# Optimization experiments

Hardware: AMD Instinct MI355X
Metric: run time of the kernel (lower is better)

The kernel has to match this reference:

```python
import jax, jax.numpy as jnp
import numpy as np

N = 50000
F = 128
E = 800000
HOP = 3
ALPHA = 0.2  # leaky relu slope


def setup_inputs() -> dict:
    key = jax.random.key(0)
    ks = jax.random.split(key, 6)
    x = jax.random.normal(ks[0], (N, F), dtype=jnp.float32)
    h0 = jax.random.normal(ks[1], (N, F), dtype=jnp.float32)
    edge_index = jax.random.randint(ks[2], (2, E), 0, N, dtype=jnp.int32)
    edge_weight = jax.random.uniform(ks[3], (E,), dtype=jnp.float32)
    # xavier-uniform-ish params
    lim_w = float(np.sqrt(6.0 / (F + F)))
    W_att = jax.random.uniform(ks[4], (F, F), dtype=jnp.float32, minval=-lim_w, maxval=lim_w)
    lim_a = 1.414 * float(np.sqrt(6.0 / (2 * F + 1)))
    a = jax.random.uniform(ks[5], (2 * F, 1), dtype=jnp.float32, minval=-lim_a, maxval=lim_a)
    temp = jnp.zeros((4,), dtype=jnp.float32)
    return {"x": x, "h0": h0, "edge_index": edge_index, "edge_weight": edge_weight,
            "W_att": W_att, "a": a, "temp": temp}


def _segment_softmax(e, rows, num_segments):
    m = jax.ops.segment_max(e, rows, num_segments=num_segments)
    m = jnp.where(jnp.isfinite(m), m, 0.0)  # guard empty rows
    ex = jnp.exp(e - m[rows])
    s = jax.ops.segment_sum(ex, rows, num_segments=num_segments)
    s = jnp.where(s > 0, s, 1.0)
    return ex / s[rows]


def reference(x, h0, edge_index, edge_weight, W_att, a, temp):
    rows, cols = edge_index[0], edge_index[1]
    # --- attention (edge-wise, never materializing dense NxN e) ---
    feat = x @ W_att                       # [N, F]
    f1 = (feat @ a[:F]).squeeze(-1)        # [N]
    f2 = (feat @ a[F:]).squeeze(-1)        # [N]
    e = f1[rows] + f2[cols]                # e[i,j] at edges
    e = jnp.where(e > 0, e, ALPHA * e)     # leaky relu
    att = _segment_softmax(e, rows, N)     # sparse row softmax values
    P = 0.5 * att
    # --- lifting bases ---
    coe = jax.nn.sigmoid(temp)
    rowsum = jax.ops.segment_sum(edge_weight * P, rows, num_segments=N)  # [N]
    update = x
    feat_prime = None
    for step in range(HOP):
        # sparse mm: U @ update
        update = jax.ops.segment_sum(att[:, None] * update[cols], rows, num_segments=N)
        feat_even = coe[0] * x + update
        feat_odd = update - feat_even * rowsum[:, None]
        feat_prime = feat_odd if step == 0 else coe[2] * feat_prime + (1.0 - coe[2]) * feat_odd
    return feat_prime
```

## Files before the change

### kernel.cpp

```cpp
#include <hip/hip_runtime.h>
#include <hip/hip_fp16.h>

#define NN 50000
#define FF 128
#define EE 800000
#define ALPHA 0.2f
#define ESHIFT 4.0f

#define NBINS 196
#define CAPB 5120
#define EPB 2048
#define NWIN 784
#define WCAP 1600

__global__ void k_w(const float* __restrict__ W, const float* __restrict__ a,
                    float* __restrict__ w12) {
    int k = threadIdx.x;
    float s1 = 0.f, s2 = 0.f;
    const float* wr = W + k * FF;
    for (int j = 0; j < FF; ++j) {
        float w = wr[j];
        s1 += w * a[j];
        s2 += w * a[FF + j];
    }
    w12[k] = s1;
    w12[FF + k] = s2;
}

__global__ void k_f(const float* __restrict__ x, const float* __restrict__ w12,
                    float* __restrict__ f1, float* __restrict__ f2,
                    __half* __restrict__ xh) {
    int gid = blockIdx.x * blockDim.x + threadIdx.x;
    int node = gid >> 6;
    int lane = threadIdx.x & 63;
    if (node >= NN) return;
    float2 xv = ((const float2*)(x + (size_t)node * FF))[lane];
    ((__half2*)(xh + (size_t)node * FF))[lane] = __float22half2_rn(xv);
    float2 w1 = ((const float2*)w12)[lane];
    float2 w2 = ((const float2*)(w12 + FF))[lane];
    float s1 = xv.x * w1.x + xv.y * w1.y;
    float s2 = xv.x * w2.x + xv.y * w2.y;
#pragma unroll
    for (int o = 32; o > 0; o >>= 1) {
        s1 += __shfl_down(s1, o);
        s2 += __shfl_down(s2, o);
    }
    if (lane == 0) { f1[node] = s1; f2[node] = s2; }
}

__global__ void k_bin(const int* __restrict__ rows, const int* __restrict__ cols,
                      const float* __restrict__ ew, const float* __restrict__ f1,
                      const float* __restrict__ f2, int* __restrict__ bin_fill,
                      int2* __restrict__ binbuf) {
    __shared__ int cnt[NBINS];
    __shared__ int gbase[NBINS];
    int tid = threadIdx.x;
    if (tid < NBINS) cnt[tid] = 0;
    __syncthreads();
    int e0 = blockIdx.x * EPB;
    int rk[8], bn[8], rc[8], pay[8];
    bool vl[8];
#pragma unroll
    for (int k = 0; k < 8; ++k) {
        int e = e0 + k * 256 + tid;
        vl[k] = e < EE;
        if (vl[k]) {
            int r = rows[e], c = cols[e];
            float v = f1[r] + f2[c];
            v = v > 0.f ? v : ALPHA * v;
            float ex = __expf(v - ESHIFT);
            union { int i; __half2 h; } p;
            p.h = __floats2half2_rn(ex, ew[e] * ex);
            pay[k] = p.i;
            rc[k] = (r << 16) | c;
            bn[k] = r >> 8;
            rk[k] = atomicAdd(&cnt[bn[k]], 1);
        }
    }
    __syncthreads();
    if (tid < NBINS) {
        int c0 = cnt[tid];
        gbase[tid] = c0 ? atomicAdd(&bin_fill[tid], c0) : 0;
    }
    __syncthreads();
#pragma unroll
    for (int k = 0; k < 8; ++k) {
        if (vl[k]) {
            int pos = gbase[bn[k]] + rk[k];
            if (pos < CAPB) binbuf[(size_t)bn[k] * CAPB + pos] = make_int2(rc[k], pay[k]);
        }
    }
}

__global__ void k_csr(const int* __restrict__ bin_fill, const int2* __restrict__ binbuf,
                      int2* __restrict__ csr, int2* __restrict__ rowinfo,
                      float2* __restrict__ rowmeta) {
    __shared__ int lfill[64];
    __shared__ int pbase[65];
    __shared__ int cursor[64];
    int tid = threadIdx.x;
    int w = blockIdx.x;
    int bin = w >> 2, q = w & 3;
    int cnt = bin_fill[bin];
    if (cnt > CAPB) cnt = CAPB;
    if (tid < 64) lfill[tid] = 0;
    __syncthreads();
    const int2* bb = binbuf + (size_t)bin * CAPB;
    for (int i = tid; i < cnt; i += 256) {
        int rl = (bb[i].x >> 16) & 0xFF;
        if ((rl >> 6) == q) atomicAdd(&lfill[rl & 63], 1);
    }
    __syncthreads();
    if (tid < 64) {
        int pc = (lfill[tid] + 7) & ~7;
        int s = pc;
#pragma unroll
        for (int o = 1; o < 64; o <<= 1) {
            int t = __shfl_up(s, o);
            if (tid >= o) s += t;
        }
        pbase[tid + 1] = s;
        if (tid == 0) pbase[0] = 0;
    }
    __syncthreads();
    int wbase = w * WCAP;
    if (tid < 64) cursor[tid] = wbase + pbase[tid];
    __syncthreads();
    for (int i = tid; i < cnt; i += 256) {
        int2 e = bb[i];
        int rl = (e.x >> 16) & 0xFF;
        if ((rl >> 6) == q) {
            int p = atomicAdd(&cursor[rl & 63], 1);
            csr[p] = make_int2(e.x & 0xFFFF, e.y);
        }
    }
    __syncthreads();
    if (tid < 64) {
        int r = (bin << 8) + (q << 6) + tid;
        if (r < NN) {
            int beg = wbase + pbase[tid];
            int dreal = lfill[tid];
            int dpad = (dreal + 7) & ~7;
            for (int p = dreal; p < dpad; ++p) csr[beg + p] = make_int2(0, 0);
            float se = 0.f, sw = 0.f;
            for (int i = 0; i < dreal; ++i) {
                union { int i32; __half2 h; } pp;
                pp.i32 = csr[beg + i].y;
                float2 e2 = __half22float2(pp.h);
                se += e2.x;
                sw += e2.y;
            }
            float inv = se > 0.f ? 1.f / se : 0.f;
            rowinfo[r] = make_int2(beg, dpad);
            rowmeta[r] = make_float2(inv, 0.5f * sw * inv);
        }
    }
}

__global__ void k_hop(const float* __restrict__ x, const __half* __restrict__ uin,
                      __half* __restrict__ uout, const int2* __restrict__ rowinfo,
                      const float2* __restrict__ rowmeta, const int2* __restrict__ csr,
                      const float* __restrict__ temp, __half* __restrict__ S,
                      float* __restrict__ out, int step) {
    int wave = threadIdx.x >> 6;
    int lane = threadIdx.x & 63;
    int r = __builtin_amdgcn_readfirstlane(blockIdx.x * 4 + wave);
    if (r >= NN) return;
    int2 ri = rowinfo[r];
    float2 mt = rowmeta[r];
    const unsigned long long* bk = (const unsigned long long*)(csr + ri.x);
    int d = ri.y;
    float ax = 0.f, ay = 0.f;
    if (d > 0) {
        unsigned long long b[8];
        __half2 h[8];
#pragma unroll
        for (int t = 0; t < 8; ++t) b[t] = __builtin_nontemporal_load(bk + t);
#pragma unroll
        for (int t = 0; t < 8; ++t) {
            int col = (int)(unsigned)b[t];
            h[t] = ((const __half2*)(uin + (size_t)col * FF))[lane];
        }
        for (int j = 8; j + 8 <= d; j += 8) {
            unsigned long long b2[8];
            __half2 h2[8];
#pragma unroll
            for (int t = 0; t < 8; ++t) b2[t] = __builtin_nontemporal_load(bk + j + t);
#pragma unroll
            for (int t = 0; t < 8; ++t) {
                int col = (int)(unsigned)b2[t];
                h2[t] = ((const __half2*)(uin + (size_t)col * FF))[lane];
            }
#pragma unroll
            for (int t = 0; t < 8; ++t) {
                union { unsigned u; __half2 h2v; } p;
                p.u = (unsigned)(b[t] >> 32);
                float att = __half2float(__low2half(p.h2v));
                float2 u = __half22float2(h[t]);
                ax += att * u.x;
                ay += att * u.y;
            }
#pragma unroll
            for (int t = 0; t < 8; ++t) { b[t] = b2[t]; h[t] = h2[t]; }
        }
#pragma unroll
        for (int t = 0; t < 8; ++t) {
            union { unsigned u; __half2 h2v; } p;
            p.u = (unsigned)(b[t] >> 32);
            float att = __half2float(__low2half(p.h2v));
            float2 u = __half22float2(h[t]);
            ax += att * u.x;
            ay += att * u.y;
        }
    }
    ax *= mt.x;
    ay *= mt.x;
    float c2 = 1.f / (1.f + __expf(-temp[2]));
    __half2* Sr = (__half2*)(S + (size_t)r * FF);
    if (step == 0) {
        ((__half2*)(uout + (size_t)r * FF))[lane] = __float22half2_rn(make_float2(ax, ay));
        float w0 = c2 * c2;
        Sr[lane] = __float22half2_rn(make_float2(w0 * ax, w0 * ay));
    } else if (step == 1) {
        ((__half2*)(uout + (size_t)r * FF))[lane] = __float22half2_rn(make_float2(ax, ay));
        float w1 = c2 * (1.f - c2);
        float2 sv = __half22float2(Sr[lane]);
        Sr[lane] = __float22half2_rn(make_float2(sv.x + w1 * ax, sv.y + w1 * ay));
    } else {
        float rs = mt.y;
        float coe0 = 1.f / (1.f + __expf(-temp[0]));
        float w2 = 1.f - c2;
        float2 sv = __half22float2(Sr[lane]);
        float2 xv = ((const float2*)(x + (size_t)r * FF))[lane];
        float k1 = 1.f - rs;
        float k2 = coe0 * rs;
        ((float2*)(out + (size_t)r * FF))[lane] =
            make_float2(k1 * (sv.x + w2 * ax) - k2 * xv.x,
                        k1 * (sv.y + w2 * ay) - k2 * xv.y);
    }
}

extern "C" void kernel_launch(void* const* d_in, const int* in_sizes, int n_in,
                              void* d_out, int out_size, void* d_ws, size_t ws_size,
                              hipStream_t stream) {
    const float* x = (const float*)d_in[0];
    const int* eidx = (const int*)d_in[2];
    const int* rows = eidx;
    const int* cols = eidx + EE;
    const float* ew = (const float*)d_in[3];
    const float* W = (const float*)d_in[4];
    const float* a = (const float*)d_in[5];
    const float* temp = (const float*)d_in[6];
    float* out = (float*)d_out;

    float* ws = (float*)d_ws;
    int* bin_fill = (int*)ws;
    float* w12 = ws + 256;
    float* f1 = ws + 512;
    float* f2 = f1 + NN;
    int2* rowinfo = (int2*)(f2 + NN);
    float2* rowmeta = (float2*)(rowinfo + NN);
    int2* csr = (int2*)(rowmeta + NN);
    __half* xh = (__half*)(csr + (size_t)NWIN * WCAP);
    __half* uh0 = xh + (size_t)NN * FF;
    __half* Sb = uh0 + (size_t)NN * FF;
    int2* binbuf = (int2*)Sb;
    __half* uh1 = xh;

    hipMemsetAsync(bin_fill, 0, NBINS * sizeof(int), stream);

    k_w<<<1, 128, 0, stream>>>(W, a, w12);
    k_f<<<(NN + 3) / 4, 256, 0, stream>>>(x, w12, f1, f2, xh);
    k_bin<<<(EE + EPB - 1) / EPB, 256, 0, stream>>>(rows, cols, ew, f1, f2, bin_fill, binbuf);
    k_csr<<<NWIN, 256, 0, stream>>>(bin_fill, binbuf, csr, rowinfo, rowmeta);
    k_hop<<<(NN + 3) / 4, 256, 0, stream>>>(x, xh, uh0, rowinfo, rowmeta, csr, temp, Sb, out, 0);
    k_hop<<<(NN + 3) / 4, 256, 0, stream>>>(x, uh0, uh1, rowinfo, rowmeta, csr, temp, Sb, out, 1);
    k_hop<<<(NN + 3) / 4, 256, 0, stream>>>(x, uh1, nullptr, rowinfo, rowmeta, csr, temp, Sb, out, 2);
}
```

Before: 248.3 us.

## Pack CSR entries into 32-bit words with prenormalized half attention

```diff
diff --git a/kernel.cpp b/kernel.cpp
--- a/kernel.cpp
+++ b/kernel.cpp
@@ -93,11 +93,12 @@
 }
 
 __global__ void k_csr(const int* __restrict__ bin_fill, const int2* __restrict__ binbuf,
-                      int2* __restrict__ csr, int2* __restrict__ rowinfo,
-                      float2* __restrict__ rowmeta) {
+                      unsigned* __restrict__ csr, int2* __restrict__ rowinfo,
+                      float* __restrict__ rowmeta) {
     __shared__ int lfill[64];
     __shared__ int pbase[65];
     __shared__ int cursor[64];
+    __shared__ int2 grouped[WCAP];
     int tid = threadIdx.x;
     int w = blockIdx.x;
     int bin = w >> 2, q = w & 3;
@@ -123,43 +124,55 @@
         if (tid == 0) pbase[0] = 0;
     }
     __syncthreads();
-    int wbase = w * WCAP;
-    if (tid < 64) cursor[tid] = wbase + pbase[tid];
+    if (tid < 64) cursor[tid] = pbase[tid];
     __syncthreads();
     for (int i = tid; i < cnt; i += 256) {
         int2 e = bb[i];
         int rl = (e.x >> 16) & 0xFF;
         if ((rl >> 6) == q) {
             int p = atomicAdd(&cursor[rl & 63], 1);
-            csr[p] = make_int2(e.x & 0xFFFF, e.y);
+            grouped[p] = e;
         }
     }
     __syncthreads();
     if (tid < 64) {
+        int lbeg = pbase[tid];
+        int dreal = lfill[tid];
+        int dpad = (dreal + 7) & ~7;
+        float se = 0.f, sw = 0.f;
+        for (int i = 0; i < dreal; ++i) {
+            union { int i32; __half2 h; } pp;
+            pp.i32 = grouped[lbeg + i].y;
+            float2 e2 = __half22float2(pp.h);
+            se += e2.x;
+            sw += e2.y;
+        }
+        float inv = se > 0.f ? 1.f / se : 0.f;
+        for (int i = 0; i < dreal; ++i) {
+            int2 en = grouped[lbeg + i];
+            union { int i32; __half2 h; } pp;
+            pp.i32 = en.y;
+            float att = __half2float(__low2half(pp.h)) * inv;
+            union { __half h; unsigned short u; } ah;
+            ah.h = __float2half_rn(att);
+            grouped[lbeg + i].x = (int)(((unsigned)ah.u << 16) | ((unsigned)en.x & 0xFFFFu));
+        }
+        for (int i = dreal; i < dpad; ++i) grouped[lbeg + i].x = 0;
         int r = (bin << 8) + (q << 6) + tid;
         if (r < NN) {
-            int beg = wbase + pbase[tid];
-            int dreal = lfill[tid];
-            int dpad = (dreal + 7) & ~7;
-            for (int p = dreal; p < dpad; ++p) csr[beg + p] = make_int2(0, 0);
-            float se = 0.f, sw = 0.f;
-            for (int i = 0; i < dreal; ++i) {
-                union { int i32; __half2 h; } pp;
-                pp.i32 = csr[beg + i].y;
-                float2 e2 = __half22float2(pp.h);
-                se += e2.x;
-                sw += e2.y;
-            }
-            float inv = se > 0.f ? 1.f / se : 0.f;
-            rowinfo[r] = make_int2(beg, dpad);
-            rowmeta[r] = make_float2(inv, 0.5f * sw * inv);
-        }
-    }
+            rowinfo[r] = make_int2(w * WCAP + lbeg, dpad);
+            rowmeta[r] = 0.5f * sw * inv;
+        }
+    }
+    __syncthreads();
+    int total = pbase[64];
+    unsigned* cb = csr + (size_t)w * WCAP;
+    for (int i = tid; i < total; i += 256) cb[i] = (unsigned)grouped[i].x;
 }
 
 __global__ void k_hop(const float* __restrict__ x, const __half* __restrict__ uin,
                       __half* __restrict__ uout, const int2* __restrict__ rowinfo,
-                      const float2* __restrict__ rowmeta, const int2* __restrict__ csr,
+                      const float* __restrict__ rowmeta, const unsigned* __restrict__ csr,
                       const float* __restrict__ temp, __half* __restrict__ S,
                       float* __restrict__ out, int step) {
     int wave = threadIdx.x >> 6;
@@ -167,54 +180,57 @@
     int r = __builtin_amdgcn_readfirstlane(blockIdx.x * 4 + wave);
     if (r >= NN) return;
     int2 ri = rowinfo[r];
-    float2 mt = rowmeta[r];
-    const unsigned long long* bk = (const unsigned long long*)(csr + ri.x);
-    int d = ri.y;
+    const unsigned long long* bk2 = (const unsigned long long*)(csr + ri.x);
+    int dq = ri.y >> 1;
     float ax = 0.f, ay = 0.f;
-    if (d > 0) {
-        unsigned long long b[8];
+    if (dq > 0) {
+        unsigned long long b[4];
         __half2 h[8];
 #pragma unroll
-        for (int t = 0; t < 8; ++t) b[t] = __builtin_nontemporal_load(bk + t);
+        for (int t = 0; t < 4; ++t) b[t] = __builtin_nontemporal_load(bk2 + t);
 #pragma unroll
         for (int t = 0; t < 8; ++t) {
-            int col = (int)(unsigned)b[t];
+            unsigned word = (t & 1) ? (unsigned)(b[t >> 1] >> 32) : (unsigned)b[t >> 1];
+            int col = word & 0xFFFF;
             h[t] = ((const __half2*)(uin + (size_t)col * FF))[lane];
         }
-        for (int j = 8; j + 8 <= d; j += 8) {
-            unsigned long long b2[8];
+        for (int j = 4; j + 4 <= dq; j += 4) {
+            unsigned long long b2[4];
             __half2 h2[8];
 #pragma unroll
-            for (int t = 0; t < 8; ++t) b2[t] = __builtin_nontemporal_load(bk + j + t);
+            for (int t = 0; t < 4; ++t) b2[t] = __builtin_nontemporal_load(bk2 + j + t);
 #pragma unroll
             for (int t = 0; t < 8; ++t) {
-                int col = (int)(unsigned)b2[t];
+                unsigned word = (t & 1) ? (unsigned)(b2[t >> 1] >> 32) : (unsigned)b2[t >> 1];
+                int col = word & 0xFFFF;
                 h2[t] = ((const __half2*)(uin + (size_t)col * FF))[lane];
             }
 #pragma unroll
             for (int t = 0; t < 8; ++t) {
-                union { unsigned u; __half2 h2v; } p;
-                p.u = (unsigned)(b[t] >> 32);
-                float att = __half2float(__low2half(p.h2v));
+                unsigned word = (t & 1) ? (unsigned)(b[t >> 1] >> 32) : (unsigned)b[t >> 1];
+                union { unsigned short u; __half hh; } ah;
+                ah.u = (unsigned short)(word >> 16);
+                float att = __half2float(ah.hh);
                 float2 u = __half22float2(h[t]);
                 ax += att * u.x;
                 ay += att * u.y;
             }
 #pragma unroll
-            for (int t = 0; t < 8; ++t) { b[t] = b2[t]; h[t] = h2[t]; }
+            for (int t = 0; t < 4; ++t) b[t] = b2[t];
+#pragma unroll
+            for (int t = 0; t < 8; ++t) h[t] = h2[t];
         }
 #pragma unroll
         for (int t = 0; t < 8; ++t) {
-            union { unsigned u; __half2 h2v; } p;
-            p.u = (unsigned)(b[t] >> 32);
-            float att = __half2float(__low2half(p.h2v));
+            unsigned word = (t & 1) ? (unsigned)(b[t >> 1] >> 32) : (unsigned)b[t >> 1];
+            union { unsigned short u; __half hh; } ah;
+            ah.u = (unsigned short)(word >> 16);
+            float att = __half2float(ah.hh);
             float2 u = __half22float2(h[t]);
             ax += att * u.x;
             ay += att * u.y;
         }
     }
-    ax *= mt.x;
-    ay *= mt.x;
     float c2 = 1.f / (1.f + __expf(-temp[2]));
     __half2* Sr = (__half2*)(S + (size_t)r * FF);
     if (step == 0) {
@@ -227,7 +243,7 @@
         float2 sv = __half22float2(Sr[lane]);
         Sr[lane] = __float22half2_rn(make_float2(sv.x + w1 * ax, sv.y + w1 * ay));
     } else {
-        float rs = mt.y;
+        float rs = rowmeta[r];
         float coe0 = 1.f / (1.f + __expf(-temp[0]));
         float w2 = 1.f - c2;
         float2 sv = __half22float2(Sr[lane]);
@@ -259,8 +275,8 @@
     float* f1 = ws + 512;
     float* f2 = f1 + NN;
     int2* rowinfo = (int2*)(f2 + NN);
-    float2* rowmeta = (float2*)(rowinfo + NN);
-    int2* csr = (int2*)(rowmeta + NN);
+    float* rowmeta = (float*)(rowinfo + NN);
+    unsigned* csr = (unsigned*)(rowmeta + NN);
     __half* xh = (__half*)(csr + (size_t)NWIN * WCAP);
     __half* uh0 = xh + (size_t)NN * FF;
     __half* Sb = uh0 + (size_t)NN * FF;
```

Result: slower. 266.1 us (+7.2%).
